# Kernel optimization log

Hardware: AMD Instinct MI355X
Metric: run time of the kernel (lower is better)

Reference implementation:

```python
import jax, jax.numpy as jnp
import numpy as np

# Dims: B=batch, C=in_ch (channels), L=pooled length, N=num_classes
B, C, L, N = 256, 2048, 512, 1000
FINAL_SHIFT = 4            # final_shift init arg
FC_SHIFT = 11              # int(log2(in_ch)) = int(log2(2048))


def dead_shift(x_i32, shift):
    # zero out values with |x| < 2^shift, then arithmetic right shift
    thr = jnp.int32(1 << shift)
    x = jnp.where(jnp.abs(x_i32) >= thr, x_i32, jnp.int32(0))
    return x >> shift  # numpy-style arithmetic shift for signed int32


def shift_clamp_i32_to_i8(x_i32, shift):
    x = dead_shift(x_i32, shift)
    return jnp.clip(x, -128, 127).astype(jnp.int8)


def setup_inputs() -> dict:
    key = jax.random.key(0)
    k1, k2 = jax.random.split(key)
    x = jax.random.randint(k1, (B, C, L), -128, 128, dtype=jnp.int32).astype(jnp.int8)
    weights = jax.random.randint(k2, (N, C), -128, 128, dtype=jnp.int32).astype(jnp.int8)
    return {"x": x, "weights": weights}


def reference(x, weights):
    # sum-pool over L: (B, C, L) -> (B, C) in int32
    acc = jnp.sum(x.astype(jnp.int32), axis=2)
    acc = dead_shift(acc, FINAL_SHIFT)
    # IntLinear: int32 matmul (same math as the torch broadcast-multiply-sum,
    # without materializing the (B, N, C) intermediate)
    w32 = weights.astype(jnp.int32)
    y = jnp.einsum('bc,nc->bn', acc, w32)  # (B, N) int32
    return shift_clamp_i32_to_i8(y, FC_SHIFT)
```

## Files before the change

### kernel.cpp

```cpp
#include <hip/hip_runtime.h>

#define BB 256
#define CC 2048
#define LL 512
#define NN 1000
#define FINAL_SHIFT 4
#define FC_SHIFT 11

#define TBB 64
#define TNN 128
#define BK 64
#define NKQ 16
#define ASTR 36
#define WSTR 132

#if __has_builtin(__builtin_amdgcn_sdot4)
#define DOT4(a, b, c) __builtin_amdgcn_sdot4((a), (b), (c), false)
#else
static __device__ __forceinline__ int dot4_fb(int a, int b, int c) {
#pragma unroll
    for (int j = 0; j < 4; ++j) {
        int av = (a << (24 - 8 * j)) >> 24;
        int bv = (b << (24 - 8 * j)) >> 24;
        c += av * bv;
    }
    return c;
}
#define DOT4(a, b, c) dot4_fb((a), (b), (c))
#endif

__device__ __forceinline__ int dead_shift_i(int x, int shift) {
    int thr = 1 << shift;
    int ax = x < 0 ? -x : x;
    x = (ax >= thr) ? x : 0;
    return x >> shift;
}

__device__ __forceinline__ int pack_hi(int4 u) {
    return ((u.x >> 6) & 255) | (((u.y >> 6) & 255) << 8) |
           (((u.z >> 6) & 255) << 16) | (((u.w >> 6) & 255) << 24);
}
__device__ __forceinline__ int pack_lo(int4 u) {
    return (u.x & 63) | ((u.y & 63) << 8) | ((u.z & 63) << 16) | ((u.w & 63) << 24);
}
__device__ __forceinline__ int pack_b(int4 u) {
    return (u.x & 255) | ((u.y & 255) << 8) | ((u.z & 255) << 16) | ((u.w & 255) << 24);
}

__global__ __launch_bounds__(256) void pool_kernel(const int* __restrict__ x,
                                                   int* __restrict__ acc) {
    int wave = threadIdx.x >> 6;
    int lane = threadIdx.x & 63;
    int g = lane >> 4;
    int j = lane & 15;
    long long rowBase = ((long long)blockIdx.x * 4 + wave) * 8;
    const int* pA = x + (rowBase + g) * (long long)LL;
    const int* pB = x + (rowBase + 4 + g) * (long long)LL;

    int4 v[8], u[8];
#pragma unroll
    for (int c = 0; c < 8; ++c) v[c] = *(const int4*)(pA + c * 64 + j * 4);
#pragma unroll
    for (int c = 0; c < 8; ++c) u[c] = *(const int4*)(pB + c * 64 + j * 4);

    int sA = 0, sB = 0;
#pragma unroll
    for (int c = 0; c < 8; ++c) sA += v[c].x + v[c].y + v[c].z + v[c].w;
#pragma unroll
    for (int c = 0; c < 8; ++c) sB += u[c].x + u[c].y + u[c].z + u[c].w;

    sA += __shfl_xor(sA, 1, 64);  sB += __shfl_xor(sB, 1, 64);
    sA += __shfl_xor(sA, 2, 64);  sB += __shfl_xor(sB, 2, 64);
    sA += __shfl_xor(sA, 4, 64);  sB += __shfl_xor(sB, 4, 64);
    sA += __shfl_xor(sA, 8, 64);  sB += __shfl_xor(sB, 8, 64);

    if (j == 0) {
        acc[rowBase + g]     = dead_shift_i(sA, FINAL_SHIFT);
        acc[rowBase + 4 + g] = dead_shift_i(sB, FINAL_SHIFT);
    }
}

__global__ __launch_bounds__(256) void gemm_kernel(const int* __restrict__ acc,
                                                   const int* __restrict__ w,
                                                   int* __restrict__ partial,
                                                   int kch) {
    __shared__ int As[TBB][ASTR];
    __shared__ int Ws[NKQ][WSTR];

    int b0 = blockIdx.x * TBB;
    int n0 = blockIdx.y * TNN;
    int kbase = blockIdx.z * kch;

    int t   = threadIdx.x;
    int tx4 = (t & 15) * 4;
    int ty4 = (t >> 4) * 4;

    int rH[4][8], rL[4][8];
#pragma unroll
    for (int bi = 0; bi < 4; ++bi)
#pragma unroll
        for (int j = 0; j < 8; ++j) { rH[bi][j] = 0; rL[bi][j] = 0; }

    for (int k0 = kbase; k0 < kbase + kch; k0 += BK) {
        {
            int b   = t >> 2;
            int kq0 = (t & 3) * 4;
            const int* src = acc + (long long)(b0 + b) * CC + k0 + kq0 * 4;
            int4 u0 = *(const int4*)(src + 0);
            int4 u1 = *(const int4*)(src + 4);
            int4 u2 = *(const int4*)(src + 8);
            int4 u3 = *(const int4*)(src + 12);
            *(int4*)&As[b][kq0]      = make_int4(pack_hi(u0), pack_hi(u1), pack_hi(u2), pack_hi(u3));
            *(int4*)&As[b][16 + kq0] = make_int4(pack_lo(u0), pack_lo(u1), pack_lo(u2), pack_lo(u3));
        }
        {
            int jq = t & 15;
            int ng = t >> 4;
#pragma unroll
            for (int rep = 0; rep < 8; ++rep) {
                int n  = rep * 16 + ng;
                int nn = n0 + n;
                int4 u = make_int4(0, 0, 0, 0);
                if (nn < NN) u = *(const int4*)(w + (long long)nn * CC + k0 + jq * 4);
                Ws[jq][n] = pack_b(u);
            }
        }
        __syncthreads();

#pragma unroll
        for (int q4 = 0; q4 < NKQ; q4 += 4) {
            int4 aH[4], aL[4];
#pragma unroll
            for (int bi = 0; bi < 4; ++bi) {
                aH[bi] = *(const int4*)&As[ty4 + bi][q4];
                aL[bi] = *(const int4*)&As[ty4 + bi][16 + q4];
            }
#pragma unroll
            for (int q = 0; q < 4; ++q) {
                int4 w0 = *(const int4*)&Ws[q4 + q][tx4];
                int4 w1 = *(const int4*)&Ws[q4 + q][64 + tx4];
#pragma unroll
                for (int bi = 0; bi < 4; ++bi) {
                    int ah = (q == 0) ? aH[bi].x : (q == 1) ? aH[bi].y
                           : (q == 2) ? aH[bi].z : aH[bi].w;
                    int al = (q == 0) ? aL[bi].x : (q == 1) ? aL[bi].y
                           : (q == 2) ? aL[bi].z : aL[bi].w;
                    rH[bi][0] = DOT4(ah, w0.x, rH[bi][0]);
                    rH[bi][1] = DOT4(ah, w0.y, rH[bi][1]);
                    rH[bi][2] = DOT4(ah, w0.z, rH[bi][2]);
                    rH[bi][3] = DOT4(ah, w0.w, rH[bi][3]);
                    rH[bi][4] = DOT4(ah, w1.x, rH[bi][4]);
                    rH[bi][5] = DOT4(ah, w1.y, rH[bi][5]);
                    rH[bi][6] = DOT4(ah, w1.z, rH[bi][6]);
                    rH[bi][7] = DOT4(ah, w1.w, rH[bi][7]);
                    rL[bi][0] = DOT4(al, w0.x, rL[bi][0]);
                    rL[bi][1] = DOT4(al, w0.y, rL[bi][1]);
                    rL[bi][2] = DOT4(al, w0.z, rL[bi][2]);
                    rL[bi][3] = DOT4(al, w0.w, rL[bi][3]);
                    rL[bi][4] = DOT4(al, w1.x, rL[bi][4]);
                    rL[bi][5] = DOT4(al, w1.y, rL[bi][5]);
                    rL[bi][6] = DOT4(al, w1.z, rL[bi][6]);
                    rL[bi][7] = DOT4(al, w1.w, rL[bi][7]);
                }
            }
        }
        __syncthreads();
    }

    long long base = (long long)blockIdx.z * BB * NN;
#pragma unroll
    for (int bi = 0; bi < 4; ++bi) {
        int b = b0 + ty4 + bi;
#pragma unroll
        for (int j = 0; j < 8; ++j) {
            int n = n0 + ((j < 4) ? (tx4 + j) : (64 + tx4 + (j - 4)));
            if (n < NN)
                partial[base + (long long)b * NN + n] = (rH[bi][j] << 6) + rL[bi][j];
        }
    }
}

__global__ __launch_bounds__(256) void epilogue_kernel(const int* __restrict__ partial,
                                                       int* __restrict__ out, int z) {
    int idx = blockIdx.x * 256 + threadIdx.x;
    if (idx >= BB * NN) return;
    int s = 0;
    for (int i = 0; i < z; ++i) s += partial[(long long)i * BB * NN + idx];
    int v = dead_shift_i(s, FC_SHIFT);
    v = min(127, max(-128, v));
    out[idx] = v;
}

extern "C" void kernel_launch(void* const* d_in, const int* in_sizes, int n_in,
                              void* d_out, int out_size, void* d_ws, size_t ws_size,
                              hipStream_t stream) {
    const int* x = (const int*)d_in[0];
    const int* w = (const int*)d_in[1];
    int* out = (int*)d_out;

    int* acc     = (int*)d_ws;
    int* partial = acc + (size_t)BB * CC;

    size_t accBytes = (size_t)BB * CC * 4;
    int Z = 8;
    while (Z > 1 && ws_size < accBytes + (size_t)Z * BB * NN * 4) Z >>= 1;
    int kch = CC / Z;

    pool_kernel<<<(BB * CC) / 32, 256, 0, stream>>>(x, acc);

    dim3 g2(BB / TBB, (NN + TNN - 1) / TNN, Z);
    gemm_kernel<<<g2, 256, 0, stream>>>(acc, w, partial, kch);

    epilogue_kernel<<<(BB * NN + 255) / 256, 256, 0, stream>>>(partial, out, Z);
}
```

Before: 226.6 us.

## Make pool kernel persistent with register prefetch and nontemporal loads

```diff
diff --git a/kernel.cpp b/kernel.cpp
--- a/kernel.cpp
+++ b/kernel.cpp
@@ -14,6 +14,12 @@
 #define ASTR 36
 #define WSTR 132
 
+#define PBLK 2048
+#define RPI  (PBLK * 32)
+#define PITER (BB * CC / RPI)
+
+typedef int v4i __attribute__((ext_vector_type(4)));
+
 #if __has_builtin(__builtin_amdgcn_sdot4)
 #define DOT4(a, b, c) __builtin_amdgcn_sdot4((a), (b), (c), false)
 #else
@@ -53,30 +59,47 @@
     int lane = threadIdx.x & 63;
     int g = lane >> 4;
     int j = lane & 15;
-    long long rowBase = ((long long)blockIdx.x * 4 + wave) * 8;
-    const int* pA = x + (rowBase + g) * (long long)LL;
-    const int* pB = x + (rowBase + 4 + g) * (long long)LL;
-
-    int4 v[8], u[8];
-#pragma unroll
-    for (int c = 0; c < 8; ++c) v[c] = *(const int4*)(pA + c * 64 + j * 4);
-#pragma unroll
-    for (int c = 0; c < 8; ++c) u[c] = *(const int4*)(pB + c * 64 + j * 4);
-
-    int sA = 0, sB = 0;
-#pragma unroll
-    for (int c = 0; c < 8; ++c) sA += v[c].x + v[c].y + v[c].z + v[c].w;
-#pragma unroll
-    for (int c = 0; c < 8; ++c) sB += u[c].x + u[c].y + u[c].z + u[c].w;
-
-    sA += __shfl_xor(sA, 1, 64);  sB += __shfl_xor(sB, 1, 64);
-    sA += __shfl_xor(sA, 2, 64);  sB += __shfl_xor(sB, 2, 64);
-    sA += __shfl_xor(sA, 4, 64);  sB += __shfl_xor(sB, 4, 64);
-    sA += __shfl_xor(sA, 8, 64);  sB += __shfl_xor(sB, 8, 64);
-
-    if (j == 0) {
-        acc[rowBase + g]     = dead_shift_i(sA, FINAL_SHIFT);
-        acc[rowBase + 4 + g] = dead_shift_i(sB, FINAL_SHIFT);
+
+    long long rb = (long long)blockIdx.x * 32 + wave * 8;
+
+    v4i v[16];
+    {
+        const int* pA = x + (rb + g) * (long long)LL + j * 4;
+        const int* pB = x + (rb + 4 + g) * (long long)LL + j * 4;
+#pragma unroll
+        for (int c = 0; c < 8; ++c) v[c]     = __builtin_nontemporal_load((const v4i*)(pA + c * 64));
+#pragma unroll
+        for (int c = 0; c < 8; ++c) v[8 + c] = __builtin_nontemporal_load((const v4i*)(pB + c * 64));
+    }
+
+#pragma unroll
+    for (int it = 0; it < PITER; ++it) {
+        int sA = 0, sB = 0;
+#pragma unroll
+        for (int c = 0; c < 8; ++c) sA += v[c].x + v[c].y + v[c].z + v[c].w;
+#pragma unroll
+        for (int c = 0; c < 8; ++c) sB += v[8 + c].x + v[8 + c].y + v[8 + c].z + v[8 + c].w;
+
+        long long rbn = rb + RPI;
+        if (it + 1 < PITER) {
+            const int* pA = x + (rbn + g) * (long long)LL + j * 4;
+            const int* pB = x + (rbn + 4 + g) * (long long)LL + j * 4;
+#pragma unroll
+            for (int c = 0; c < 8; ++c) v[c]     = __builtin_nontemporal_load((const v4i*)(pA + c * 64));
+#pragma unroll
+            for (int c = 0; c < 8; ++c) v[8 + c] = __builtin_nontemporal_load((const v4i*)(pB + c * 64));
+        }
+
+        sA += __shfl_xor(sA, 1, 64);  sB += __shfl_xor(sB, 1, 64);
+        sA += __shfl_xor(sA, 2, 64);  sB += __shfl_xor(sB, 2, 64);
+        sA += __shfl_xor(sA, 4, 64);  sB += __shfl_xor(sB, 4, 64);
+        sA += __shfl_xor(sA, 8, 64);  sB += __shfl_xor(sB, 8, 64);
+
+        if (j == 0) {
+            acc[rb + g]     = dead_shift_i(sA, FINAL_SHIFT);
+            acc[rb + 4 + g] = dead_shift_i(sB, FINAL_SHIFT);
+        }
+        rb = rbn;
     }
 }
 
@@ -206,7 +229,7 @@
     while (Z > 1 && ws_size < accBytes + (size_t)Z * BB * NN * 4) Z >>= 1;
     int kch = CC / Z;
 
-    pool_kernel<<<(BB * CC) / 32, 256, 0, stream>>>(x, acc);
+    pool_kernel<<<PBLK, 256, 0, stream>>>(x, acc);
 
     dim3 g2(BB / TBB, (NN + TNN - 1) / TNN, Z);
     gemm_kernel<<<g2, 256, 0, stream>>>(acc, w, partial, kch);
```

New measurement: 205.3 us. -9.4%, faster.

## Make pool kernel persistent with software-pipelined nontemporal loads

Applied to the files above, without the earlier changes.

```diff
diff --git a/kernel.cpp b/kernel.cpp
--- a/kernel.cpp
+++ b/kernel.cpp
@@ -14,6 +14,12 @@
 #define ASTR 36
 #define WSTR 132
 
+#define PBLK 2048
+#define RPS  (PBLK * 16)
+#define PITER (BB * CC / RPS)
+
+typedef int v4i __attribute__((ext_vector_type(4)));
+
 #if __has_builtin(__builtin_amdgcn_sdot4)
 #define DOT4(a, b, c) __builtin_amdgcn_sdot4((a), (b), (c), false)
 #else
@@ -47,36 +53,42 @@
     return (u.x & 255) | ((u.y & 255) << 8) | ((u.z & 255) << 16) | ((u.w & 255) << 24);
 }
 
-__global__ __launch_bounds__(256) void pool_kernel(const int* __restrict__ x,
-                                                   int* __restrict__ acc) {
+__global__ __launch_bounds__(256, 8) void pool_kernel(const int* __restrict__ x,
+                                                      int* __restrict__ acc) {
     int wave = threadIdx.x >> 6;
     int lane = threadIdx.x & 63;
     int g = lane >> 4;
     int j = lane & 15;
-    long long rowBase = ((long long)blockIdx.x * 4 + wave) * 8;
-    const int* pA = x + (rowBase + g) * (long long)LL;
-    const int* pB = x + (rowBase + 4 + g) * (long long)LL;
-
-    int4 v[8], u[8];
-#pragma unroll
-    for (int c = 0; c < 8; ++c) v[c] = *(const int4*)(pA + c * 64 + j * 4);
-#pragma unroll
-    for (int c = 0; c < 8; ++c) u[c] = *(const int4*)(pB + c * 64 + j * 4);
-
-    int sA = 0, sB = 0;
-#pragma unroll
-    for (int c = 0; c < 8; ++c) sA += v[c].x + v[c].y + v[c].z + v[c].w;
-#pragma unroll
-    for (int c = 0; c < 8; ++c) sB += u[c].x + u[c].y + u[c].z + u[c].w;
-
-    sA += __shfl_xor(sA, 1, 64);  sB += __shfl_xor(sB, 1, 64);
-    sA += __shfl_xor(sA, 2, 64);  sB += __shfl_xor(sB, 2, 64);
-    sA += __shfl_xor(sA, 4, 64);  sB += __shfl_xor(sB, 4, 64);
-    sA += __shfl_xor(sA, 8, 64);  sB += __shfl_xor(sB, 8, 64);
-
-    if (j == 0) {
-        acc[rowBase + g]     = dead_shift_i(sA, FINAL_SHIFT);
-        acc[rowBase + 4 + g] = dead_shift_i(sB, FINAL_SHIFT);
+
+    long long rb = (long long)blockIdx.x * 16 + wave * 4;
+
+    v4i v[8];
+    {
+        const int* p = x + (rb + g) * (long long)LL + j * 4;
+#pragma unroll
+        for (int c = 0; c < 8; ++c) v[c] = __builtin_nontemporal_load((const v4i*)(p + c * 64));
+    }
+
+#pragma unroll
+    for (int it = 0; it < PITER; ++it) {
+        int s = 0;
+#pragma unroll
+        for (int c = 0; c < 8; ++c) s += v[c].x + v[c].y + v[c].z + v[c].w;
+
+        long long rbn = rb + RPS;
+        if (it + 1 < PITER) {
+            const int* p = x + (rbn + g) * (long long)LL + j * 4;
+#pragma unroll
+            for (int c = 0; c < 8; ++c) v[c] = __builtin_nontemporal_load((const v4i*)(p + c * 64));
+        }
+
+        s += __shfl_xor(s, 1, 64);
+        s += __shfl_xor(s, 2, 64);
+        s += __shfl_xor(s, 4, 64);
+        s += __shfl_xor(s, 8, 64);
+
+        if (j == 0) acc[rb + g] = dead_shift_i(s, FINAL_SHIFT);
+        rb = rbn;
     }
 }
 
@@ -206,7 +218,7 @@
     while (Z > 1 && ws_size < accBytes + (size_t)Z * BB * NN * 4) Z >>= 1;
     int kch = CC / Z;
 
-    pool_kernel<<<(BB * CC) / 32, 256, 0, stream>>>(x, acc);
+    pool_kernel<<<PBLK, 256, 0, stream>>>(x, acc);
 
     dim3 g2(BB / TBB, (NN + TNN - 1) / TNN, Z);
     gemm_kernel<<<g2, 256, 0, stream>>>(acc, w, partial, kch);
```

New measurement: 199.8 us, median of 2. 1.13x faster.
